# Kernel optimization log

Hardware: AMD Instinct MI355X
Metric: run time of the kernel (lower is better)

## Reference

```python
import jax, jax.numpy as jnp
import numpy as np

N = 50000        # nodes
E = 1_600_000    # edges
F = 128          # dataset_num_features (== dim so layer weights stack)
D = 128          # hidden_dim
L = 3            # num_gc_layers
G = 512          # graphs in batch
BN_EPS = 1e-5


def setup_inputs() -> dict:
    key = jax.random.key(0)
    ks = jax.random.split(key, 12)
    s = 0.05
    x = jax.random.normal(ks[0], (N, F), jnp.float32)
    edge_index = jax.random.randint(ks[1], (2, E), 0, N)
    batch = jnp.sort(jax.random.randint(ks[2], (N,), 0, G))
    # GIN MLP per layer: Linear(F->D), ReLU, Linear(D->D)  (F==D so stackable)
    W1 = jax.random.normal(ks[3], (L, F, D), jnp.float32) * s
    b1 = jnp.zeros((L, D), jnp.float32)
    W2 = jax.random.normal(ks[4], (L, D, D), jnp.float32) * s
    b2 = jnp.zeros((L, D), jnp.float32)
    bn_gamma = jnp.ones((L, D), jnp.float32)
    bn_beta = jnp.zeros((L, D), jnp.float32)
    # proj_head: Linear(3D->3D), ReLU, Linear(3D->3D)
    ED = L * D
    Wp1 = jax.random.normal(ks[5], (ED, ED), jnp.float32) * s
    bp1 = jnp.zeros((ED,), jnp.float32)
    Wp2 = jax.random.normal(ks[6], (ED, ED), jnp.float32) * s
    bp2 = jnp.zeros((ED,), jnp.float32)
    return {"x": x, "edge_index": edge_index, "batch": batch,
            "W1": W1, "b1": b1, "W2": W2, "b2": b2,
            "bn_gamma": bn_gamma, "bn_beta": bn_beta,
            "Wp1": Wp1, "bp1": bp1, "Wp2": Wp2, "bp2": bp2}


def reference(x, edge_index, batch, W1, b1, W2, b2, bn_gamma, bn_beta, Wp1, bp1, Wp2, bp2):
    src, dst = edge_index[0], edge_index[1]
    h = x
    xs = []
    for i in range(L):
        # GINConv (eps=0): nn(x_i + sum_{j->i} x_j) via gather + scatter-add
        agg = jax.ops.segment_sum(h[src], dst, num_segments=N)  # [N, D]
        m = agg + h
        m = jax.nn.relu(m @ W1[i] + b1[i])
        m = m @ W2[i] + b2[i]
        m = jax.nn.relu(m)                 # outer F.relu in Encoder.forward
        # BatchNorm1d (training mode, biased variance)
        mu = m.mean(axis=0)
        var = m.var(axis=0)
        h = (m - mu) * jax.lax.rsqrt(var + BN_EPS) * bn_gamma[i] + bn_beta[i]
        xs.append(h)
    node = jnp.concatenate(xs, axis=1)                    # [N, L*D]
    pooled = jax.ops.segment_sum(node, batch, num_segments=G)  # global_add_pool [G, L*D]
    z = jax.nn.relu(pooled @ Wp1 + bp1) @ Wp2 + bp2       # proj_head
    return z
```

## Files before the change

### kernel.cpp

```cpp
#include <hip/hip_runtime.h>

#define NN 50000
#define NE 1600000
#define GG 512
#define PAD 96
#define NBKT 196
#define BCAP 12288
#define CHUNK 6250
#define NBLK_MLP 782
#define NRED1 196
#define BN_EPS 1e-5f
#define XCONV_TOT (NN * 32)
#define NTRB 96

typedef __attribute__((ext_vector_type(8))) short short8;
typedef __attribute__((ext_vector_type(4))) float f32x4;

__device__ __forceinline__ unsigned short f2bf(float x) {
    unsigned int u = __builtin_bit_cast(unsigned int, x);
    return (unsigned short)((u + 0x7FFFu + ((u >> 16) & 1u)) >> 16);
}
__device__ __forceinline__ float bf2f(unsigned int b) {
    return __builtin_bit_cast(float, b << 16);
}

__global__ __launch_bounds__(256) void bucket_k(const int* __restrict__ src, const int* __restrict__ dst,
                                                int* __restrict__ bcur, unsigned int* __restrict__ staging) {
    __shared__ int hist[NBKT];
    __shared__ int curs[NBKT];
    const int t = threadIdx.x;
    if (t < NBKT) hist[t] = 0;
    __syncthreads();
    const int e0 = blockIdx.x * CHUNK;
    const int e1 = e0 + CHUNK;
    for (int e = e0 + t; e < e1; e += 256) atomicAdd(&hist[dst[e] >> 8], 1);
    __syncthreads();
    if (t < NBKT) {
        int c = hist[t];
        curs[t] = (c > 0) ? atomicAdd(&bcur[t], c) : 0;
    }
    __syncthreads();
    for (int e = e0 + t; e < e1; e += 256) {
        int d = dst[e];
        int b = d >> 8;
        int pos = atomicAdd(&curs[b], 1);
        staging[(size_t)b * BCAP + pos] = (unsigned int)(d & 255) | ((unsigned int)src[e] << 8);
    }
}

__global__ __launch_bounds__(256) void ellfill_k(const int* __restrict__ bcur,
                                                 const unsigned int* __restrict__ staging,
                                                 int* __restrict__ cnt, unsigned short* __restrict__ ell) {
    __shared__ unsigned short lell[256 * PAD];
    __shared__ int lcnt[256];
    const int b = blockIdx.x, t = threadIdx.x;
    lcnt[t] = 0;
    __syncthreads();
    const int tot = bcur[b];
    const unsigned int* sg = staging + (size_t)b * BCAP;
    for (int i = t; i < tot; i += 256) {
        unsigned int v = sg[i];
        int r = v & 255;
        int p = atomicAdd(&lcnt[r], 1);
        lell[r * PAD + p] = (unsigned short)(v >> 8);
    }
    __syncthreads();
    const int n0 = b << 8;
    const int nrows = min(256, NN - n0);
    for (int i = t; i < nrows * 12; i += 256) {
        int r = i / 12, q = i % 12;
        *(uint4*)(ell + (size_t)(n0 + r) * PAD + q * 8) = *(const uint4*)(lell + r * PAD + q * 8);
    }
    if (t < nrows) cnt[n0 + t] = lcnt[t];
}

__global__ __launch_bounds__(256) void conv_k(const float* __restrict__ x,
                                              const float* __restrict__ W1, const float* __restrict__ W2,
                                              const float* __restrict__ Wp1, const float* __restrict__ Wp2,
                                              unsigned short* __restrict__ xb, unsigned short* __restrict__ Wt,
                                              unsigned short* __restrict__ Wpt, int* __restrict__ bcur) {
    const int b = blockIdx.x, tid = threadIdx.x;
    if (b < NTRB) {
        __shared__ float tile[64 * 65];
        const float* S;
        unsigned short* D;
        int srcW, dstW, k0, c0;
        if (b < 24) {
            int mat = b >> 2, t = b & 3;
            S = ((mat & 1) ? W2 : W1) + (size_t)(mat >> 1) * 16384;
            D = Wt + (size_t)mat * 16384;
            srcW = 128; dstW = 128;
            k0 = (t >> 1) * 64; c0 = (t & 1) * 64;
        } else {
            int bb = b - 24;
            int mat = bb / 36, t = bb % 36;
            S = mat ? Wp2 : Wp1;
            D = Wpt + (size_t)mat * 147456;
            srcW = 384; dstW = 384;
            k0 = (t / 6) * 64; c0 = (t % 6) * 64;
        }
        for (int idx = tid; idx < 4096; idx += 256) {
            int r = idx >> 6, c = idx & 63;
            tile[r * 65 + c] = S[(size_t)(k0 + r) * srcW + c0 + c];
        }
        __syncthreads();
        for (int idx = tid; idx < 4096; idx += 256) {
            int r = idx >> 6, c = idx & 63;
            D[(size_t)(c0 + r) * dstW + k0 + c] = f2bf(tile[c * 65 + r]);
        }
    } else {
        int i = (b - NTRB) * 256 + tid;
        if (i < NBKT) bcur[i] = 0;
        const int stp = (gridDim.x - NTRB) * 256;
        for (; i < XCONV_TOT; i += stp) {
            float4 v = ((const float4*)x)[i];
            uint2 pk;
            pk.x = (unsigned int)f2bf(v.x) | ((unsigned int)f2bf(v.y) << 16);
            pk.y = (unsigned int)f2bf(v.z) | ((unsigned int)f2bf(v.w) << 16);
            ((uint2*)xb)[i] = pk;
        }
    }
}

__global__ __launch_bounds__(256) void layer_k(const int* __restrict__ cnt, const unsigned short* __restrict__ ell,
                                               const unsigned short* __restrict__ h, const float* __restrict__ ss,
                                               const unsigned short* __restrict__ Wt,
                                               const float* __restrict__ bias1, const float* __restrict__ bias2,
                                               unsigned short* __restrict__ yb, float* __restrict__ scr) {
    __shared__ __align__(16) unsigned short sW[128 * 136];
    __shared__ __align__(16) unsigned short sA[64 * 136];
    float* sred = (float*)sA;
    const int tid = threadIdx.x;
    const int row0 = blockIdx.x * 64;
    for (int ch = tid; ch < 2048; ch += 256) {
        int c = ch >> 4, i = ch & 15;
        *(uint4*)(sW + c * 136 + i * 8) = *(const uint4*)(Wt + c * 128 + i * 8);
    }
    {
        const int l = tid & 15;
        float sc[8], sh[8];
        #pragma unroll
        for (int j = 0; j < 8; ++j) { sc[j] = 1.f; sh[j] = 0.f; }
        if (ss) {
            #pragma unroll
            for (int j = 0; j < 8; ++j) { sc[j] = ss[l * 8 + j]; sh[j] = ss[128 + l * 8 + j]; }
        }
        #pragma unroll
        for (int pass = 0; pass < 4; ++pass) {
            int lrow = pass * 16 + (tid >> 4);
            int n = row0 + lrow;
            uint4 pk = {0u, 0u, 0u, 0u};
            if (n < NN) {
                int e = cnt[n];
                const unsigned short* row = ell + (size_t)n * PAD;
                float acc[8];
                {
                    uint4 q = *(const uint4*)(h + (size_t)n * 128 + l * 8);
                    unsigned int qq[4] = {q.x, q.y, q.z, q.w};
                    #pragma unroll
                    for (int j = 0; j < 4; ++j) {
                        acc[2 * j]     = bf2f(qq[j] & 0xffffu) * sc[2 * j];
                        acc[2 * j + 1] = bf2f(qq[j] >> 16)     * sc[2 * j + 1];
                    }
                }
                int i = 0;
                for (; i + 8 <= e; i += 8) {
                    uint4 ip = *(const uint4*)(row + i);
                    int s0 = ip.x & 0xffff, s1 = ip.x >> 16, s2 = ip.y & 0xffff, s3 = ip.y >> 16;
                    int s4 = ip.z & 0xffff, s5 = ip.z >> 16, s6 = ip.w & 0xffff, s7 = ip.w >> 16;
                    uint4 q0 = *(const uint4*)(h + (size_t)s0 * 128 + l * 8);
                    uint4 q1 = *(const uint4*)(h + (size_t)s1 * 128 + l * 8);
                    uint4 q2 = *(const uint4*)(h + (size_t)s2 * 128 + l * 8);
                    uint4 q3 = *(const uint4*)(h + (size_t)s3 * 128 + l * 8);
                    uint4 q4 = *(const uint4*)(h + (size_t)s4 * 128 + l * 8);
                    uint4 q5 = *(const uint4*)(h + (size_t)s5 * 128 + l * 8);
                    uint4 q6 = *(const uint4*)(h + (size_t)s6 * 128 + l * 8);
                    uint4 q7 = *(const uint4*)(h + (size_t)s7 * 128 + l * 8);
                    unsigned int a0[4] = {q0.x, q0.y, q0.z, q0.w};
                    unsigned int a1[4] = {q1.x, q1.y, q1.z, q1.w};
                    unsigned int a2[4] = {q2.x, q2.y, q2.z, q2.w};
                    unsigned int a3[4] = {q3.x, q3.y, q3.z, q3.w};
                    unsigned int a4[4] = {q4.x, q4.y, q4.z, q4.w};
                    unsigned int a5[4] = {q5.x, q5.y, q5.z, q5.w};
                    unsigned int a6[4] = {q6.x, q6.y, q6.z, q6.w};
                    unsigned int a7[4] = {q7.x, q7.y, q7.z, q7.w};
                    #pragma unroll
                    for (int j = 0; j < 4; ++j) {
                        float t0 = bf2f(a0[j] & 0xffffu) + bf2f(a1[j] & 0xffffu);
                        float t1 = bf2f(a2[j] & 0xffffu) + bf2f(a3[j] & 0xffffu);
                        float t2 = bf2f(a4[j] & 0xffffu) + bf2f(a5[j] & 0xffffu);
                        float t3 = bf2f(a6[j] & 0xffffu) + bf2f(a7[j] & 0xffffu);
                        acc[2*j] = fmaf((t0 + t1) + (t2 + t3), sc[2*j], acc[2*j]);
                        float u0 = bf2f(a0[j] >> 16) + bf2f(a1[j] >> 16);
                        float u1 = bf2f(a2[j] >> 16) + bf2f(a3[j] >> 16);
                        float u2 = bf2f(a4[j] >> 16) + bf2f(a5[j] >> 16);
                        float u3 = bf2f(a6[j] >> 16) + bf2f(a7[j] >> 16);
                        acc[2*j+1] = fmaf((u0 + u1) + (u2 + u3), sc[2*j+1], acc[2*j+1]);
                    }
                }
                for (; i < e; ++i) {
                    int s0 = row[i];
                    uint4 q = *(const uint4*)(h + (size_t)s0 * 128 + l * 8);
                    unsigned int qq[4] = {q.x, q.y, q.z, q.w};
                    #pragma unroll
                    for (int j = 0; j < 4; ++j) {
                        acc[2*j]   = fmaf(bf2f(qq[j] & 0xffffu), sc[2*j],   acc[2*j]);
                        acc[2*j+1] = fmaf(bf2f(qq[j] >> 16),     sc[2*j+1], acc[2*j+1]);
                    }
                }
                float fe = (float)(e + 1);
                #pragma unroll
                for (int j = 0; j < 8; ++j) acc[j] = fmaf(fe, sh[j], acc[j]);
                pk.x = (unsigned int)f2bf(acc[0]) | ((unsigned int)f2bf(acc[1]) << 16);
                pk.y = (unsigned int)f2bf(acc[2]) | ((unsigned int)f2bf(acc[3]) << 16);
                pk.z = (unsigned int)f2bf(acc[4]) | ((unsigned int)f2bf(acc[5]) << 16);
                pk.w = (unsigned int)f2bf(acc[6]) | ((unsigned int)f2bf(acc[7]) << 16);
            }
            *(uint4*)(sA + lrow * 136 + l * 8) = pk;
        }
    }
    __syncthreads();
    const int w = tid >> 6, l = tid & 63;
    const int lr = l & 15, lk = l >> 4;
    const unsigned short* ap = sA + (w * 16 + lr) * 136 + lk * 8;
    short8 af0 = *(const short8*)(ap);
    short8 af1 = *(const short8*)(ap + 32);
    short8 af2 = *(const short8*)(ap + 64);
    short8 af3 = *(const short8*)(ap + 96);
    __syncthreads();
    f32x4 acc[8] = {};
    #pragma unroll
    for (int c = 0; c < 8; ++c) {
        const unsigned short* wp = sW + (c * 16 + lr) * 136 + lk * 8;
        short8 wf0 = *(const short8*)(wp);
        short8 wf1 = *(const short8*)(wp + 32);
        short8 wf2 = *(const short8*)(wp + 64);
        short8 wf3 = *(const short8*)(wp + 96);
        acc[c] = __builtin_amdgcn_mfma_f32_16x16x32_bf16(af0, wf0, acc[c], 0, 0, 0);
        acc[c] = __builtin_amdgcn_mfma_f32_16x16x32_bf16(af1, wf1, acc[c], 0, 0, 0);
        acc[c] = __builtin_amdgcn_mfma_f32_16x16x32_bf16(af2, wf2, acc[c], 0, 0, 0);
        acc[c] = __builtin_amdgcn_mfma_f32_16x16x32_bf16(af3, wf3, acc[c], 0, 0, 0);
    }
    const int lrow = w * 16 + lk * 4;
    #pragma unroll
    for (int c = 0; c < 8; ++c) {
        int col = c * 16 + lr;
        float b = bias1[col];
        #pragma unroll
        for (int r = 0; r < 4; ++r) {
            float v = fmaxf(acc[c][r] + b, 0.f);
            sA[(lrow + r) * 136 + col] = f2bf(v);
        }
    }
    __syncthreads();
    for (int ch = tid; ch < 2048; ch += 256) {
        int c = ch >> 4, i = ch & 15;
        *(uint4*)(sW + c * 136 + i * 8) = *(const uint4*)(Wt + 16384 + c * 128 + i * 8);
    }
    const unsigned short* tp = sA + (w * 16 + lr) * 136 + lk * 8;
    short8 bf0 = *(const short8*)(tp);
    short8 bf1 = *(const short8*)(tp + 32);
    short8 bf2_ = *(const short8*)(tp + 64);
    short8 bf3 = *(const short8*)(tp + 96);
    f32x4 acc2[8] = {};
    __syncthreads();
    #pragma unroll
    for (int c = 0; c < 8; ++c) {
        const unsigned short* wp = sW + (c * 16 + lr) * 136 + lk * 8;
        short8 wf0 = *(const short8*)(wp);
        short8 wf1 = *(const short8*)(wp + 32);
        short8 wf2 = *(const short8*)(wp + 64);
        short8 wf3 = *(const short8*)(wp + 96);
        acc2[c] = __builtin_amdgcn_mfma_f32_16x16x32_bf16(bf0, wf0, acc2[c], 0, 0, 0);
        acc2[c] = __builtin_amdgcn_mfma_f32_16x16x32_bf16(bf1, wf1, acc2[c], 0, 0, 0);
        acc2[c] = __builtin_amdgcn_mfma_f32_16x16x32_bf16(bf2_, wf2, acc2[c], 0, 0, 0);
        acc2[c] = __builtin_amdgcn_mfma_f32_16x16x32_bf16(bf3, wf3, acc2[c], 0, 0, 0);
    }
    const int drow = row0 + lk * 4 + w * 16;
    #pragma unroll
    for (int c = 0; c < 8; ++c) {
        int col = c * 16 + lr;
        float b = bias2[col];
        float s1 = 0.f, s2 = 0.f;
        #pragma unroll
        for (int r = 0; r < 4; ++r) {
            int grow = drow + r;
            float v = fmaxf(acc2[c][r] + b, 0.f);
            if (grow < NN) {
                yb[(size_t)grow * 128 + col] = f2bf(v);
                s1 += v;
                s2 += v * v;
            }
        }
        s1 += __shfl_xor(s1, 16); s1 += __shfl_xor(s1, 32);
        s2 += __shfl_xor(s2, 16); s2 += __shfl_xor(s2, 32);
        if (lk == 0) {
            sred[((w * 16 + lr) * 8 + c) * 2 + 0] = s1;
            sred[((w * 16 + lr) * 8 + c) * 2 + 1] = s2;
        }
    }
    __syncthreads();
    int st = tid & 1, c = (tid >> 1) & 7, lr2 = tid >> 4;
    float t = 0.f;
    #pragma unroll
    for (int w2 = 0; w2 < 4; ++w2) t += sred[((w2 * 16 + lr2) * 8 + c) * 2 + st];
    scr[(size_t)blockIdx.x * 256 + st * 128 + c * 16 + lr2] = t;
}

__global__ __launch_bounds__(256) void bnr1_k(const float* __restrict__ scr, float* __restrict__ part) {
    int b = blockIdx.x, d = threadIdx.x;
    float a = 0.f;
    for (int r = b; r < NBLK_MLP; r += NRED1) a += scr[(size_t)r * 256 + d];
    part[(size_t)b * 256 + d] = a;
}

__global__ __launch_bounds__(1024) void bnr2_k(const float* __restrict__ part, const float* __restrict__ gamma,
                                               const float* __restrict__ beta, float* __restrict__ ss) {
    __shared__ float red[4][256];
    int t = threadIdx.x, q = t >> 8, d = t & 255;
    float a = 0.f;
    for (int r = q; r < NRED1; r += 4) a += part[(size_t)r * 256 + d];
    red[q][d] = a;
    __syncthreads();
    if (t < 256) red[0][t] = red[0][t] + red[1][t] + red[2][t] + red[3][t];
    __syncthreads();
    if (t < 128) {
        float mu = red[0][t] * (1.0f / NN);
        float var = red[0][128 + t] * (1.0f / NN) - mu * mu;
        float sc = gamma[t] * rsqrtf(var + BN_EPS);
        ss[t] = sc;
        ss[128 + t] = beta[t] - mu * sc;
    }
}

__global__ __launch_bounds__(128) void pool_k(const unsigned short* __restrict__ y0,
                                              const unsigned short* __restrict__ y1,
                                              const unsigned short* __restrict__ y2,
                                              const float* __restrict__ ss,
                                              const int* __restrict__ batch, unsigned short* __restrict__ pb) {
    int g = blockIdx.x;
    int lo = 0, hi = NN;
    while (lo < hi) { int mid = (lo + hi) >> 1; if (batch[mid] < g) lo = mid + 1; else hi = mid; }
    int s = lo;
    lo = s; hi = NN;
    while (lo < hi) { int mid = (lo + hi) >> 1; if (batch[mid] < g + 1) lo = mid + 1; else hi = mid; }
    int e = lo;
    int t = threadIdx.x;
    float sc0 = ss[t],       sh0 = ss[128 + t];
    float sc1 = ss[256 + t], sh1 = ss[384 + t];
    float sc2 = ss[512 + t], sh2 = ss[640 + t];
    float a0 = 0.f, a1 = 0.f, a2 = 0.f;
    for (int n = s; n < e; ++n) {
        a0 += fmaf(bf2f((unsigned int)y0[(size_t)n * 128 + t]), sc0, sh0);
        a1 += fmaf(bf2f((unsigned int)y1[(size_t)n * 128 + t]), sc1, sh1);
        a2 += fmaf(bf2f((unsigned int)y2[(size_t)n * 128 + t]), sc2, sh2);
    }
    pb[(size_t)g * 384 + t]       = f2bf(a0);
    pb[(size_t)g * 384 + t + 128] = f2bf(a1);
    pb[(size_t)g * 384 + t + 256] = f2bf(a2);
}

__global__ __launch_bounds__(256) void projm_k(const unsigned short* __restrict__ A,
                                               const unsigned short* __restrict__ Wpt,
                                               const float* __restrict__ bias,
                                               unsigned short* __restrict__ outb,
                                               float* __restrict__ outf) {
    __shared__ __align__(16) unsigned short sW[128 * 136];
    const int tid = threadIdx.x;
    const int col_off = blockIdx.y * 128;
    const int w = tid >> 6, l = tid & 63;
    const int lr = l & 15, lk = l >> 4;
    const int row0 = blockIdx.x * 64 + w * 16;
    f32x4 acc[8] = {};
    for (int kk = 0; kk < 3; ++kk) {
        __syncthreads();
        for (int ch = tid; ch < 2048; ch += 256) {
            int c = ch >> 4, i = ch & 15;
            *(uint4*)(sW + c * 136 + i * 8) = *(const uint4*)(Wpt + (size_t)(col_off + c) * 384 + kk * 128 + i * 8);
        }
        const unsigned short* ap = A + (size_t)(row0 + lr) * 384 + kk * 128 + lk * 8;
        short8 af0 = *(const short8*)(ap);
        short8 af1 = *(const short8*)(ap + 32);
        short8 af2 = *(const short8*)(ap + 64);
        short8 af3 = *(const short8*)(ap + 96);
        __syncthreads();
        #pragma unroll
        for (int c = 0; c < 8; ++c) {
            const unsigned short* wp = sW + (c * 16 + lr) * 136 + lk * 8;
            short8 wf0 = *(const short8*)(wp);
            short8 wf1 = *(const short8*)(wp + 32);
            short8 wf2 = *(const short8*)(wp + 64);
            short8 wf3 = *(const short8*)(wp + 96);
            acc[c] = __builtin_amdgcn_mfma_f32_16x16x32_bf16(af0, wf0, acc[c], 0, 0, 0);
            acc[c] = __builtin_amdgcn_mfma_f32_16x16x32_bf16(af1, wf1, acc[c], 0, 0, 0);
            acc[c] = __builtin_amdgcn_mfma_f32_16x16x32_bf16(af2, wf2, acc[c], 0, 0, 0);
            acc[c] = __builtin_amdgcn_mfma_f32_16x16x32_bf16(af3, wf3, acc[c], 0, 0, 0);
        }
    }
    const int drow = row0 + lk * 4;
    #pragma unroll
    for (int c = 0; c < 8; ++c) {
        int col = col_off + c * 16 + lr;
        float b = bias[col];
        #pragma unroll
        for (int r = 0; r < 4; ++r) {
            float v = acc[c][r] + b;
            if (outb) outb[(size_t)(drow + r) * 384 + col] = f2bf(fmaxf(v, 0.f));
            else      outf[(size_t)(drow + r) * 384 + col] = v;
        }
    }
}

extern "C" void kernel_launch(void* const* d_in, const int* in_sizes, int n_in,
                              void* d_out, int out_size, void* d_ws, size_t ws_size,
                              hipStream_t stream) {
    const float* x     = (const float*)d_in[0];
    const int*   ei    = (const int*)d_in[1];
    const int*   srcI  = ei;
    const int*   dstI  = ei + NE;
    const int*   batch = (const int*)d_in[2];
    const float* W1    = (const float*)d_in[3];
    const float* b1    = (const float*)d_in[4];
    const float* W2    = (const float*)d_in[5];
    const float* b2    = (const float*)d_in[6];
    const float* gamma = (const float*)d_in[7];
    const float* beta  = (const float*)d_in[8];
    const float* Wp1   = (const float*)d_in[9];
    const float* bp1   = (const float*)d_in[10];
    const float* Wp2   = (const float*)d_in[11];
    const float* bp2   = (const float*)d_in[12];
    float* out = (float*)d_out;

    float* ssbuf  = (float*)d_ws;
    float* part   = ssbuf + 3 * 256;
    float* scr    = part + NRED1 * 256;
    int*   cnt    = (int*)(scr + 3 * NBLK_MLP * 256);
    int*   bcur   = cnt + NN;
    unsigned int* staging = (unsigned int*)(bcur + NBKT + 4);
    unsigned short* ell  = (unsigned short*)(staging + (size_t)NBKT * BCAP);
    unsigned short* xb   = ell + (size_t)NN * PAD;
    unsigned short* yb0  = xb + (size_t)NN * 128;
    unsigned short* yb1  = yb0 + (size_t)NN * 128;
    unsigned short* yb2  = yb1 + (size_t)NN * 128;
    unsigned short* Wt   = yb2 + (size_t)NN * 128;
    unsigned short* Wpt  = Wt + 6 * 16384;
    unsigned short* pb   = Wpt + 2 * 147456;
    unsigned short* z1b  = pb + (size_t)GG * 384;

    conv_k<<<NTRB + 1024, 256, 0, stream>>>(x, W1, W2, Wp1, Wp2, xb, Wt, Wpt, bcur);
    bucket_k<<<256, 256, 0, stream>>>(srcI, dstI, bcur, staging);
    ellfill_k<<<NBKT, 256, 0, stream>>>(bcur, staging, cnt, ell);

    unsigned short* ybufs[3] = {yb0, yb1, yb2};
    for (int l = 0; l < 3; ++l) {
        const unsigned short* h = (l == 0) ? xb : ybufs[l - 1];
        const float* ssl        = (l == 0) ? nullptr : (ssbuf + (l - 1) * 256);

        layer_k<<<NBLK_MLP, 256, 0, stream>>>(cnt, ell, h, ssl,
                                              Wt + (size_t)(2 * l) * 16384,
                                              b1 + l * 128, b2 + l * 128,
                                              ybufs[l], scr + (size_t)l * NBLK_MLP * 256);
        bnr1_k<<<NRED1, 256, 0, stream>>>(scr + (size_t)l * NBLK_MLP * 256, part);
        bnr2_k<<<1, 1024, 0, stream>>>(part, gamma + l * 128, beta + l * 128, ssbuf + l * 256);
    }

    pool_k<<<GG, 128, 0, stream>>>(yb0, yb1, yb2, ssbuf, batch, pb);
    {
        dim3 gp(8, 3);
        projm_k<<<gp, 256, 0, stream>>>(pb, Wpt, bp1, z1b, nullptr);
        projm_k<<<gp, 256, 0, stream>>>(z1b, Wpt + 147456, bp2, nullptr, out);
    }
}
```

Measured before the change: 505.8 us.

## Split fused aggregate+MLP layer kernel into separate gather and MFMA kernels

The fused layer kernel, which did the neighbor gather-sum and then the two-layer MFMA MLP out of shared memory, becomes two kernels. A new LDS-free agg_k does the ELL gather into a global bf16 buffer with one node per 16 threads. mlp_k then loads its A fragments directly from that buffer. The aim is more waves in flight to hide latency on the memory-bound gather, which the fused kernel's large shared-memory footprint had limited. The cost is an extra global write and read of the aggregated activations per layer and one more kernel launch per layer.

Measured after the change: 444.0 us. 12.2% less time.

```diff
diff --git a/kernel.cpp b/kernel.cpp
--- a/kernel.cpp
+++ b/kernel.cpp
@@ -122,113 +122,111 @@
     }
 }
 
-__global__ __launch_bounds__(256) void layer_k(const int* __restrict__ cnt, const unsigned short* __restrict__ ell,
-                                               const unsigned short* __restrict__ h, const float* __restrict__ ss,
-                                               const unsigned short* __restrict__ Wt,
-                                               const float* __restrict__ bias1, const float* __restrict__ bias2,
-                                               unsigned short* __restrict__ yb, float* __restrict__ scr) {
+__global__ __launch_bounds__(256) void agg_k(const int* __restrict__ cnt, const unsigned short* __restrict__ ell,
+                                             const unsigned short* __restrict__ h, const float* __restrict__ ss,
+                                             unsigned short* __restrict__ m) {
+    int gid = blockIdx.x * 256 + threadIdx.x;
+    int n = gid >> 4, l = gid & 15;
+    if (n >= NN) return;
+    float sc[8], sh[8];
+    #pragma unroll
+    for (int j = 0; j < 8; ++j) { sc[j] = 1.f; sh[j] = 0.f; }
+    if (ss) {
+        #pragma unroll
+        for (int j = 0; j < 8; ++j) { sc[j] = ss[l * 8 + j]; sh[j] = ss[128 + l * 8 + j]; }
+    }
+    int e = cnt[n];
+    const unsigned short* row = ell + (size_t)n * PAD;
+    float acc[8];
+    {
+        uint4 q = *(const uint4*)(h + (size_t)n * 128 + l * 8);
+        unsigned int qq[4] = {q.x, q.y, q.z, q.w};
+        #pragma unroll
+        for (int j = 0; j < 4; ++j) {
+            acc[2 * j]     = bf2f(qq[j] & 0xffffu) * sc[2 * j];
+            acc[2 * j + 1] = bf2f(qq[j] >> 16)     * sc[2 * j + 1];
+        }
+    }
+    int i = 0;
+    for (; i + 8 <= e; i += 8) {
+        uint4 ip = *(const uint4*)(row + i);
+        int s0 = ip.x & 0xffff, s1 = ip.x >> 16, s2 = ip.y & 0xffff, s3 = ip.y >> 16;
+        int s4 = ip.z & 0xffff, s5 = ip.z >> 16, s6 = ip.w & 0xffff, s7 = ip.w >> 16;
+        uint4 q0 = *(const uint4*)(h + (size_t)s0 * 128 + l * 8);
+        uint4 q1 = *(const uint4*)(h + (size_t)s1 * 128 + l * 8);
+        uint4 q2 = *(const uint4*)(h + (size_t)s2 * 128 + l * 8);
+        uint4 q3 = *(const uint4*)(h + (size_t)s3 * 128 + l * 8);
+        uint4 q4 = *(const uint4*)(h + (size_t)s4 * 128 + l * 8);
+        uint4 q5 = *(const uint4*)(h + (size_t)s5 * 128 + l * 8);
+        uint4 q6 = *(const uint4*)(h + (size_t)s6 * 128 + l * 8);
+        uint4 q7 = *(const uint4*)(h + (size_t)s7 * 128 + l * 8);
+        unsigned int a0[4] = {q0.x, q0.y, q0.z, q0.w};
+        unsigned int a1[4] = {q1.x, q1.y, q1.z, q1.w};
+        unsigned int a2[4] = {q2.x, q2.y, q2.z, q2.w};
+        unsigned int a3[4] = {q3.x, q3.y, q3.z, q3.w};
+        unsigned int a4[4] = {q4.x, q4.y, q4.z, q4.w};
+        unsigned int a5[4] = {q5.x, q5.y, q5.z, q5.w};
+        unsigned int a6[4] = {q6.x, q6.y, q6.z, q6.w};
+        unsigned int a7[4] = {q7.x, q7.y, q7.z, q7.w};
+        #pragma unroll
+        for (int j = 0; j < 4; ++j) {
+            float t0 = bf2f(a0[j] & 0xffffu) + bf2f(a1[j] & 0xffffu);
+            float t1 = bf2f(a2[j] & 0xffffu) + bf2f(a3[j] & 0xffffu);
+            float t2 = bf2f(a4[j] & 0xffffu) + bf2f(a5[j] & 0xffffu);
+            float t3 = bf2f(a6[j] & 0xffffu) + bf2f(a7[j] & 0xffffu);
+            acc[2*j] = fmaf((t0 + t1) + (t2 + t3), sc[2*j], acc[2*j]);
+            float u0 = bf2f(a0[j] >> 16) + bf2f(a1[j] >> 16);
+            float u1 = bf2f(a2[j] >> 16) + bf2f(a3[j] >> 16);
+            float u2 = bf2f(a4[j] >> 16) + bf2f(a5[j] >> 16);
+            float u3 = bf2f(a6[j] >> 16) + bf2f(a7[j] >> 16);
+            acc[2*j+1] = fmaf((u0 + u1) + (u2 + u3), sc[2*j+1], acc[2*j+1]);
+        }
+    }
+    for (; i < e; ++i) {
+        int s0 = row[i];
+        uint4 q = *(const uint4*)(h + (size_t)s0 * 128 + l * 8);
+        unsigned int qq[4] = {q.x, q.y, q.z, q.w};
+        #pragma unroll
+        for (int j = 0; j < 4; ++j) {
+            acc[2*j]   = fmaf(bf2f(qq[j] & 0xffffu), sc[2*j],   acc[2*j]);
+            acc[2*j+1] = fmaf(bf2f(qq[j] >> 16),     sc[2*j+1], acc[2*j+1]);
+        }
+    }
+    float fe = (float)(e + 1);
+    #pragma unroll
+    for (int j = 0; j < 8; ++j) acc[j] = fmaf(fe, sh[j], acc[j]);
+    uint4 pk;
+    pk.x = (unsigned int)f2bf(acc[0]) | ((unsigned int)f2bf(acc[1]) << 16);
+    pk.y = (unsigned int)f2bf(acc[2]) | ((unsigned int)f2bf(acc[3]) << 16);
+    pk.z = (unsigned int)f2bf(acc[4]) | ((unsigned int)f2bf(acc[5]) << 16);
+    pk.w = (unsigned int)f2bf(acc[6]) | ((unsigned int)f2bf(acc[7]) << 16);
+    *(uint4*)(m + (size_t)n * 128 + l * 8) = pk;
+}
+
+__global__ __launch_bounds__(256) void mlp_k(const unsigned short* __restrict__ A,
+                                             const unsigned short* __restrict__ Wt,
+                                             const float* __restrict__ bias1,
+                                             const float* __restrict__ bias2,
+                                             unsigned short* __restrict__ yb,
+                                             float* __restrict__ scr) {
     __shared__ __align__(16) unsigned short sW[128 * 136];
-    __shared__ __align__(16) unsigned short sA[64 * 136];
-    float* sred = (float*)sA;
+    __shared__ __align__(16) unsigned short sT[64 * 136];
+    float* sred = (float*)sT;
     const int tid = threadIdx.x;
-    const int row0 = blockIdx.x * 64;
     for (int ch = tid; ch < 2048; ch += 256) {
         int c = ch >> 4, i = ch & 15;
         *(uint4*)(sW + c * 136 + i * 8) = *(const uint4*)(Wt + c * 128 + i * 8);
     }
-    {
-        const int l = tid & 15;
-        float sc[8], sh[8];
-        #pragma unroll
-        for (int j = 0; j < 8; ++j) { sc[j] = 1.f; sh[j] = 0.f; }
-        if (ss) {
-            #pragma unroll
-            for (int j = 0; j < 8; ++j) { sc[j] = ss[l * 8 + j]; sh[j] = ss[128 + l * 8 + j]; }
-        }
-        #pragma unroll
-        for (int pass = 0; pass < 4; ++pass) {
-            int lrow = pass * 16 + (tid >> 4);
-            int n = row0 + lrow;
-            uint4 pk = {0u, 0u, 0u, 0u};
-            if (n < NN) {
-                int e = cnt[n];
-                const unsigned short* row = ell + (size_t)n * PAD;
-                float acc[8];
-                {
-                    uint4 q = *(const uint4*)(h + (size_t)n * 128 + l * 8);
-                    unsigned int qq[4] = {q.x, q.y, q.z, q.w};
-                    #pragma unroll
-                    for (int j = 0; j < 4; ++j) {
-                        acc[2 * j]     = bf2f(qq[j] & 0xffffu) * sc[2 * j];
-                        acc[2 * j + 1] = bf2f(qq[j] >> 16)     * sc[2 * j + 1];
-                    }
-                }
-                int i = 0;
-                for (; i + 8 <= e; i += 8) {
-                    uint4 ip = *(const uint4*)(row + i);
-                    int s0 = ip.x & 0xffff, s1 = ip.x >> 16, s2 = ip.y & 0xffff, s3 = ip.y >> 16;
-                    int s4 = ip.z & 0xffff, s5 = ip.z >> 16, s6 = ip.w & 0xffff, s7 = ip.w >> 16;
-                    uint4 q0 = *(const uint4*)(h + (size_t)s0 * 128 + l * 8);
-                    uint4 q1 = *(const uint4*)(h + (size_t)s1 * 128 + l * 8);
-                    uint4 q2 = *(const uint4*)(h + (size_t)s2 * 128 + l * 8);
-                    uint4 q3 = *(const uint4*)(h + (size_t)s3 * 128 + l * 8);
-                    uint4 q4 = *(const uint4*)(h + (size_t)s4 * 128 + l * 8);
-                    uint4 q5 = *(const uint4*)(h + (size_t)s5 * 128 + l * 8);
-                    uint4 q6 = *(const uint4*)(h + (size_t)s6 * 128 + l * 8);
-                    uint4 q7 = *(const uint4*)(h + (size_t)s7 * 128 + l * 8);
-                    unsigned int a0[4] = {q0.x, q0.y, q0.z, q0.w};
-                    unsigned int a1[4] = {q1.x, q1.y, q1.z, q1.w};
-                    unsigned int a2[4] = {q2.x, q2.y, q2.z, q2.w};
-                    unsigned int a3[4] = {q3.x, q3.y, q3.z, q3.w};
-                    unsigned int a4[4] = {q4.x, q4.y, q4.z, q4.w};
-                    unsigned int a5[4] = {q5.x, q5.y, q5.z, q5.w};
-                    unsigned int a6[4] = {q6.x, q6.y, q6.z, q6.w};
-                    unsigned int a7[4] = {q7.x, q7.y, q7.z, q7.w};
-                    #pragma unroll
-                    for (int j = 0; j < 4; ++j) {
-                        float t0 = bf2f(a0[j] & 0xffffu) + bf2f(a1[j] & 0xffffu);
-                        float t1 = bf2f(a2[j] & 0xffffu) + bf2f(a3[j] & 0xffffu);
-                        float t2 = bf2f(a4[j] & 0xffffu) + bf2f(a5[j] & 0xffffu);
-                        float t3 = bf2f(a6[j] & 0xffffu) + bf2f(a7[j] & 0xffffu);
-                        acc[2*j] = fmaf((t0 + t1) + (t2 + t3), sc[2*j], acc[2*j]);
-                        float u0 = bf2f(a0[j] >> 16) + bf2f(a1[j] >> 16);
-                        float u1 = bf2f(a2[j] >> 16) + bf2f(a3[j] >> 16);
-                        float u2 = bf2f(a4[j] >> 16) + bf2f(a5[j] >> 16);
-                        float u3 = bf2f(a6[j] >> 16) + bf2f(a7[j] >> 16);
-                        acc[2*j+1] = fmaf((u0 + u1) + (u2 + u3), sc[2*j+1], acc[2*j+1]);
-                    }
-                }
-                for (; i < e; ++i) {
-                    int s0 = row[i];
-                    uint4 q = *(const uint4*)(h + (size_t)s0 * 128 + l * 8);
-                    unsigned int qq[4] = {q.x, q.y, q.z, q.w};
-                    #pragma unroll
-                    for (int j = 0; j < 4; ++j) {
-                        acc[2*j]   = fmaf(bf2f(qq[j] & 0xffffu), sc[2*j],   acc[2*j]);
-                        acc[2*j+1] = fmaf(bf2f(qq[j] >> 16),     sc[2*j+1], acc[2*j+1]);
-                    }
-                }
-                float fe = (float)(e + 1);
-                #pragma unroll
-                for (int j = 0; j < 8; ++j) acc[j] = fmaf(fe, sh[j], acc[j]);
-                pk.x = (unsigned int)f2bf(acc[0]) | ((unsigned int)f2bf(acc[1]) << 16);
-                pk.y = (unsigned int)f2bf(acc[2]) | ((unsigned int)f2bf(acc[3]) << 16);
-                pk.z = (unsigned int)f2bf(acc[4]) | ((unsigned int)f2bf(acc[5]) << 16);
-                pk.w = (unsigned int)f2bf(acc[6]) | ((unsigned int)f2bf(acc[7]) << 16);
-            }
-            *(uint4*)(sA + lrow * 136 + l * 8) = pk;
-        }
-    }
-    __syncthreads();
     const int w = tid >> 6, l = tid & 63;
     const int lr = l & 15, lk = l >> 4;
-    const unsigned short* ap = sA + (w * 16 + lr) * 136 + lk * 8;
+    const int row0 = blockIdx.x * 64 + w * 16;
+    const unsigned short* ap = A + (size_t)(row0 + lr) * 128 + lk * 8;
     short8 af0 = *(const short8*)(ap);
     short8 af1 = *(const short8*)(ap + 32);
     short8 af2 = *(const short8*)(ap + 64);
     short8 af3 = *(const short8*)(ap + 96);
-    __syncthreads();
     f32x4 acc[8] = {};
+    __syncthreads();
     #pragma unroll
     for (int c = 0; c < 8; ++c) {
         const unsigned short* wp = sW + (c * 16 + lr) * 136 + lk * 8;
@@ -249,7 +247,7 @@
         #pragma unroll
         for (int r = 0; r < 4; ++r) {
             float v = fmaxf(acc[c][r] + b, 0.f);
-            sA[(lrow + r) * 136 + col] = f2bf(v);
+            sT[(lrow + r) * 136 + col] = f2bf(v);
         }
     }
     __syncthreads();
@@ -257,7 +255,7 @@
         int c = ch >> 4, i = ch & 15;
         *(uint4*)(sW + c * 136 + i * 8) = *(const uint4*)(Wt + 16384 + c * 128 + i * 8);
     }
-    const unsigned short* tp = sA + (w * 16 + lr) * 136 + lk * 8;
+    const unsigned short* tp = sT + (w * 16 + lr) * 136 + lk * 8;
     short8 bf0 = *(const short8*)(tp);
     short8 bf1 = *(const short8*)(tp + 32);
     short8 bf2_ = *(const short8*)(tp + 64);
@@ -276,7 +274,7 @@
         acc2[c] = __builtin_amdgcn_mfma_f32_16x16x32_bf16(bf2_, wf2, acc2[c], 0, 0, 0);
         acc2[c] = __builtin_amdgcn_mfma_f32_16x16x32_bf16(bf3, wf3, acc2[c], 0, 0, 0);
     }
-    const int drow = row0 + lk * 4 + w * 16;
+    const int drow = row0 + lk * 4;
     #pragma unroll
     for (int c = 0; c < 8; ++c) {
         int col = c * 16 + lr;
@@ -442,7 +440,8 @@
     unsigned short* yb0  = xb + (size_t)NN * 128;
     unsigned short* yb1  = yb0 + (size_t)NN * 128;
     unsigned short* yb2  = yb1 + (size_t)NN * 128;
-    unsigned short* Wt   = yb2 + (size_t)NN * 128;
+    unsigned short* m_bf = yb2 + (size_t)NN * 128;
+    unsigned short* Wt   = m_bf + (size_t)NN * 128;
     unsigned short* Wpt  = Wt + 6 * 16384;
     unsigned short* pb   = Wpt + 2 * 147456;
     unsigned short* z1b  = pb + (size_t)GG * 384;
@@ -456,10 +455,10 @@
         const unsigned short* h = (l == 0) ? xb : ybufs[l - 1];
         const float* ssl        = (l == 0) ? nullptr : (ssbuf + (l - 1) * 256);
 
-        layer_k<<<NBLK_MLP, 256, 0, stream>>>(cnt, ell, h, ssl,
-                                              Wt + (size_t)(2 * l) * 16384,
-                                              b1 + l * 128, b2 + l * 128,
-                                              ybufs[l], scr + (size_t)l * NBLK_MLP * 256);
+        agg_k<<<3125, 256, 0, stream>>>(cnt, ell, h, ssl, m_bf);
+        mlp_k<<<NBLK_MLP, 256, 0, stream>>>(m_bf, Wt + (size_t)(2 * l) * 16384,
+                                            b1 + l * 128, b2 + l * 128,
+                                            ybufs[l], scr + (size_t)l * NBLK_MLP * 256);
         bnr1_k<<<NRED1, 256, 0, stream>>>(scr + (size_t)l * NBLK_MLP * 256, part);
         bnr2_k<<<1, 1024, 0, stream>>>(part, gamma + l * 128, beta + l * 128, ssbuf + l * 256);
     }
```
